# Kernel tuning notes

Measured on AMD Instinct MI355X. Metric: run time of the kernel, lower is better.

Reference implementation:

```python
import jax, jax.numpy as jnp
import numpy as np

# ---- static configuration (matches init_kwargs) ----
B = 8; CIN = 3; COUT = 3
H_IN, W_IN = 128, 256          # img_size
H, W = 32, 64                  # internal grid = img_size / scale_factor
E = 256; HID = 512             # embed_dim, mlp hidden (ratio 2)
NR, NPHI = 3, 4                # DISCO kernel_shape
K = 1 + (NR - 1) * NPHI        # 9 piecewise-linear basis functions
LMAX = MMAX = H                # SHT truncation on internal grid
PI = np.pi

# ---- DISCO basis: psi[k, ho, hi, dlon] (quadrature folded in), stored as conj(rfft) over lon ----
def _build_psi(nlat_in, nlon_in, nlat_out, cutoff):
    ti = PI * (np.arange(nlat_in) + 0.5) / nlat_in
    to = PI * (np.arange(nlat_out) + 0.5) / nlat_out
    ph = 2 * PI * np.arange(nlon_in) / nlon_in
    cto, sto = np.cos(to)[:, None, None], np.sin(to)[:, None, None]
    cti, sti = np.cos(ti)[None, :, None], np.sin(ti)[None, :, None]
    cph, sph = np.cos(ph)[None, None, :], np.sin(ph)[None, None, :]
    r = np.arccos(np.clip(cto * cti + sto * sti * cph, -1.0, 1.0))      # great-circle dist
    alpha = np.arctan2(sti * sph, cti * sto - sti * cto * cph)          # azimuth
    dr = cutoff / (NR - 1); dphi = 2 * PI / NPHI
    quad = (sti * (PI / nlat_in) * (2 * PI / nlon_in)) * (r <= cutoff)  # quadrature * cutoff mask
    psi = np.empty((K, nlat_out, nlat_in, nlon_in), np.float32)
    psi[0] = np.clip(1 - r / dr, 0, 1) * quad                           # isotropic center basis
    for j in range(1, NR):
        tr = np.clip(1 - np.abs(r - j * dr) / dr, 0, 1)
        for k in range(NPHI):
            d = np.abs(np.mod(alpha - k * dphi + PI, 2 * PI) - PI)
            psi[1 + (j - 1) * NPHI + k] = tr * np.clip(1 - d / dphi, 0, 1) * quad
    return np.conj(np.fft.rfft(psi, axis=-1)).astype(np.complex64)

PSIH_ENC = jnp.asarray(_build_psi(H_IN, W_IN, H, 4 * PI / (H - 1)))
PSIH_INT = jnp.asarray(_build_psi(H, W, H, 4 * (NR + 1) * PI / (H - 1)))
PSIH_DEC = jnp.asarray(_build_psi(H_IN, W_IN, H_IN, 4 * PI / (H - 1)))

# ---- normalized associated Legendre for SHT on internal equiangular grid ----
def _legendre(lmax, theta):
    ct, st = np.cos(theta), np.sin(theta)
    P = np.zeros((lmax, lmax, theta.size))
    P[0, 0] = 1.0 / np.sqrt(2.0)
    for m in range(1, lmax):
        P[m, m] = np.sqrt((2 * m + 1) / (2.0 * m)) * st * P[m - 1, m - 1]
    for m in range(lmax - 1):
        P[m + 1, m] = np.sqrt(2 * m + 3.0) * ct * P[m, m]
    for m in range(lmax):
        for l in range(m + 2, lmax):
            a = np.sqrt((4.0 * l * l - 1) / (l * l - m * m))
            b = a * np.sqrt(((l - 1.0) ** 2 - m * m) / (4.0 * (l - 1) ** 2 - 1))
            P[l, m] = a * ct * P[l - 1, m] - b * P[l - 2, m]
    return P  # [l, m, h]

_THETA = PI * (np.arange(H) + 0.5) / H
_P = _legendre(LMAX, _THETA).astype(np.float32)
PW = jnp.asarray(_P * (np.sin(_THETA) * (PI / H))[None, None, :])  # analysis (with quadrature)
PT = jnp.asarray(_P)                                                # synthesis

# ---- bilinear resample (32,64)->(128,256), periodic in lon ----
_fi = np.clip((np.arange(H_IN) + 0.5) * H / H_IN - 0.5, 0, H - 1)
LAT_I0 = jnp.asarray(np.floor(_fi).astype(np.int32))
LAT_I1 = jnp.asarray(np.minimum(np.floor(_fi).astype(np.int32) + 1, H - 1))
LAT_W = jnp.asarray((_fi - np.floor(_fi)).astype(np.float32))
_fj = np.arange(W_IN) * W / W_IN
LON_J0 = jnp.asarray((np.floor(_fj).astype(np.int32)) % W)
LON_J1 = jnp.asarray((np.floor(_fj).astype(np.int32) + 1) % W)
LON_W = jnp.asarray((_fj - np.floor(_fj)).astype(np.float32))


def _disco(x, psih, n_in, stride):
    # circular cross-correlation over lon via FFT: z[b,c,k,ho,wo]
    Xh = jnp.fft.rfft(x, axis=-1)
    Zh = jnp.einsum('khim,bcim->bckhm', psih, Xh)
    return jnp.fft.irfft(Zh, n=n_in, axis=-1)[..., ::stride]


def _spectral(x, w):
    # driscoll-healy spectral conv: per-l channel mixing in SH space
    Xh = jnp.fft.rfft(x, axis=-1)[..., :MMAX]
    c = jnp.einsum('lmh,bchm->bclm', PW, Xh)
    c = jnp.einsum('ocl,bclm->bolm', w, c)
    Xo = jnp.einsum('lmh,bolm->bohm', PT, c)
    Xo = jnp.pad(Xo, ((0, 0), (0, 0), (0, 0), (0, W // 2 + 1 - MMAX)))
    return jnp.fft.irfft(Xo, n=W, axis=-1)


def _resample(x):
    a = jnp.take(x, LAT_I0, axis=2) * (1 - LAT_W)[:, None] + jnp.take(x, LAT_I1, axis=2) * LAT_W[:, None]
    return jnp.take(a, LON_J0, axis=3) * (1 - LON_W) + jnp.take(a, LON_J1, axis=3) * LON_W


def _forward(x, enc_w, lconv_w, gconv_w, mlp_w1, mlp_b1, mlp_w2, mlp_b2, skip_w, skip_b, dec_w):
    # encoder: DISCO conv (128,256)->(32,64), CIN->E
    z = _disco(x, PSIH_ENC, W_IN, W_IN // W)          # [B,CIN,K,32,64]
    x = jnp.einsum('ock,bckhw->bohw', enc_w, z)       # [B,E,32,64]
    for i in range(4):
        res = x
        if i % 2 == 0:  # local DISCO block
            z = _disco(x, PSIH_INT, W, 1)
            x = jnp.einsum('ock,bckhw->bohw', lconv_w[i // 2], z)
        else:           # global spectral (SHT) block
            x = _spectral(x, gconv_w[i // 2])
        # MLP (1x1 convs) + linear outer skip (norm = Identity)
        h = jax.nn.relu(jnp.einsum('oc,bchw->bohw', mlp_w1[i], x) + mlp_b1[i][:, None, None])
        x = jnp.einsum('oc,bchw->bohw', mlp_w2[i], h) + mlp_b2[i][:, None, None]
        x = x + jnp.einsum('oc,bchw->bohw', skip_w[i], res) + skip_b[i][:, None, None]
    # decoder: bilinear upsample then DISCO conv at full res, E->COUT (mix channels first: COUT small)
    x = _resample(x)                                  # [B,E,128,256]
    u = jnp.einsum('ock,bchw->bokhw', dec_w, x)       # [B,COUT,K,128,256]
    Uh = jnp.fft.rfft(u, axis=-1)
    Yh = jnp.einsum('khim,bokim->bohm', PSIH_DEC, Uh)
    return jnp.fft.irfft(Yh, n=W_IN, axis=-1)         # [B,COUT,128,256]


def setup_inputs() -> dict:
    key = jax.random.key(0)
    ks = jax.random.split(key, 8)
    f = jnp.float32
    return dict(
        x=jax.random.normal(ks[0], (B, CIN, H_IN, W_IN), f),
        enc_w=jax.random.normal(ks[1], (E, CIN, K), f) * float(1 / np.sqrt(CIN * K)),
        lconv_w=jax.random.normal(ks[2], (2, E, E, K), f) * float(1 / np.sqrt(E * K)),
        gconv_w=jax.random.normal(ks[3], (2, E, E, LMAX), f) * float(1 / np.sqrt(E)),
        mlp_w1=jax.random.normal(ks[4], (4, HID, E), f) * float(np.sqrt(2.0 / E)),
        mlp_b1=jnp.zeros((4, HID), f),
        mlp_w2=jax.random.normal(ks[5], (4, E, HID), f) * float(1 / np.sqrt(HID)),
        mlp_b2=jnp.zeros((4, E), f),
        skip_w=jax.random.normal(ks[6], (4, E, E), f) * float(np.sqrt(0.5 / E)),
        skip_b=jnp.zeros((4, E), f),
        dec_w=jax.random.normal(ks[7], (COUT, E, K), f) * float(1 / np.sqrt(E * K)),
    )


def reference(x, enc_w, lconv_w, gconv_w, mlp_w1, mlp_b1, mlp_w2, mlp_b2, skip_w, skip_b, dec_w):
    return _forward(x, enc_w, lconv_w, gconv_w, mlp_w1, mlp_b1, mlp_w2, mlp_b2, skip_w, skip_b, dec_w)
```

## Files before the change

### kernel.cpp

```cpp
#include <hip/hip_runtime.h>
#include <math.h>
#include <utility>

#define DI __device__ __forceinline__

namespace {

typedef unsigned short u16;
typedef unsigned int u32;
using f16x8 = __attribute__((ext_vector_type(8))) _Float16;
using f32x4 = __attribute__((ext_vector_type(4))) float;

constexpr int BB  = 8;
constexpr int CIN = 3;
constexpr int HIN = 128, WIN = 256;
constexpr int EE  = 256;
constexpr int NSP = BB * 32 * 64;
constexpr double PI_D = 3.14159265358979323846;
constexpr int ME_ENC = 5120, ME_INT = 2048, ME_DEC = 4608;
constexpr int HW_E = 34;

DI u16 f16rne(float x) { _Float16 h = (_Float16)x; return __builtin_bit_cast(unsigned short, h); }
DI float f16tof(u16 u) { return (float)__builtin_bit_cast(_Float16, u); }
DI u32 packhl(float v) {
  u16 h = f16rne(v);
  u16 l = f16rne(v - f16tof(h));
  return (u32)h | ((u32)l << 16);
}

DI bool psi_point(int nlat_in, int nlon_in, int nlat_out, double cutoff,
                  int ho, int hi, int d, bool wantv, float* out9)
{
  double ti = PI_D * (hi + 0.5) / nlat_in;
  double to = PI_D * (ho + 0.5) / nlat_out;
  double ph = 2.0 * PI_D * d / nlon_in;
  double cto = cos(to), sto = sin(to);
  double cti = cos(ti), sti = sin(ti);
  double cph = cos(ph), sph = sin(ph);
  double ca = cto * cti + sto * sti * cph;
  ca = fmin(1.0, fmax(-1.0, ca));
  double r = acos(ca);
  if (r > cutoff) return false;
  if (wantv) {
    double dr   = cutoff * 0.5;
    double dphi = PI_D * 0.5;
    double quad = sti * (PI_D / nlat_in) * (2.0 * PI_D / nlon_in);
    out9[0] = (float)(fmin(1.0, fmax(0.0, 1.0 - r / dr)) * quad);
    double alpha = atan2(sti * sph, cti * sto - sti * cto * cph);
#pragma unroll
    for (int j = 1; j <= 2; ++j) {
      double tr = fmin(1.0, fmax(0.0, 1.0 - fabs(r - j * dr) / dr));
#pragma unroll
      for (int k2 = 0; k2 < 4; ++k2) {
        double xx = alpha - k2 * dphi + PI_D;
        double yy = xx - 2.0 * PI_D * floor(xx / (2.0 * PI_D));
        double dd = fabs(yy - PI_D);
        out9[1 + (j - 1) * 4 + k2] = (float)(tr * fmin(1.0, fmax(0.0, 1.0 - dd / dphi)) * quad);
      }
    }
  }
  return true;
}

__global__ void k_psi_count(int nlat_in, int nlon_in, int nlat_out, double cutoff, int* cnt)
{
  int hi = blockIdx.x, ho = blockIdx.y, d = threadIdx.x;
  float dummy[9];
  bool in = psi_point(nlat_in, nlon_in, nlat_out, cutoff, ho, hi, d, false, dummy);
  unsigned long long mask = __ballot(in);
  if ((threadIdx.x & 63) == 0) {
    int tot = __popcll(mask);
    if (tot) atomicAdd(cnt + ho * nlat_in + hi, tot);
  }
}

__global__ void k_psi_scan(int nlat_in, int maxe, int* cnt, int* offs)
{
  int ho = blockIdx.x;
  int* c = cnt + ho * nlat_in;
  int* o = offs + ho * (nlat_in + 1);
  int run = 0;
  for (int hi = 0; hi < nlat_in; ++hi) {
    o[hi] = run < maxe ? run : maxe;
    run += c[hi];
    c[hi] = 0;
  }
  o[nlat_in] = run < maxe ? run : maxe;
}

__global__ void k_psi_fill(int nlat_in, int nlon_in, int nlat_out, double cutoff,
                           int maxe, int* cnt, const int* __restrict__ offs, float* __restrict__ tab)
{
  int hi = blockIdx.x, ho = blockIdx.y, d = threadIdx.x;
  float p9[9];
  bool in = psi_point(nlat_in, nlon_in, nlat_out, cutoff, ho, hi, d, true, p9);
  unsigned long long mask = __ballot(in);
  int lane = threadIdx.x & 63;
  int tot = __popcll(mask);
  int wbase = 0;
  if (lane == 0 && tot) wbase = atomicAdd(cnt + ho * nlat_in + hi, tot);
  wbase = __shfl(wbase, 0, 64);
  if (in) {
    int rank = __popcll(mask & ((1ull << lane) - 1ull));
    int idx = offs[ho * (nlat_in + 1) + hi] + wbase + rank;
    if (idx < maxe) {
      float* te = tab + ((size_t)ho * maxe + idx) * 12;
      te[0] = __int_as_float((hi << 16) | d);
#pragma unroll
      for (int k = 0; k < 9; ++k) te[1 + k] = p9[k];
      te[10] = 0.f; te[11] = 0.f;
    }
  }
}

__global__ void k_legendre(float* __restrict__ PW, float* __restrict__ PT)
{
  int h = threadIdx.x;
  if (h >= 32) return;
  double th = PI_D * (h + 0.5) / 32.0;
  double ct = cos(th), st = sin(th);
  double quad = st * (PI_D / 32.0);
  double diag = 0.70710678118654752440;
  for (int m = 0; m < 32; ++m) {
    if (m > 0) diag = sqrt((2.0 * m + 1.0) / (2.0 * m)) * st * diag;
    double plm2 = diag;
    PT[((size_t)m * 32 + m) * 32 + h] = (float)plm2;
    PW[((size_t)m * 32 + m) * 32 + h] = (float)(plm2 * quad);
    if (m + 1 < 32) {
      double plm1 = sqrt(2.0 * m + 3.0) * ct * diag;
      PT[((size_t)(m + 1) * 32 + m) * 32 + h] = (float)plm1;
      PW[((size_t)(m + 1) * 32 + m) * 32 + h] = (float)(plm1 * quad);
      for (int l = m + 2; l < 32; ++l) {
        double a  = sqrt((4.0 * l * l - 1.0) / ((double)l * l - (double)m * m));
        double bb = a * sqrt((((double)(l - 1) * (l - 1)) - (double)m * m) /
                             (4.0 * (double)(l - 1) * (l - 1) - 1.0));
        double p = a * ct * plm1 - bb * plm2;
        PT[((size_t)l * 32 + m) * 32 + h] = (float)p;
        PW[((size_t)l * 32 + m) * 32 + h] = (float)(p * quad);
        plm2 = plm1; plm1 = p;
      }
    }
    for (int l = 0; l < m; ++l) {
      PT[((size_t)l * 32 + m) * 32 + h] = 0.f;
      PW[((size_t)l * 32 + m) * 32 + h] = 0.f;
    }
  }
}

__global__ void k_tw2(float* tc256, float* ts256, float* tc64, float* ts64)
{
  int t = threadIdx.x;
  double th = 2.0 * PI_D * t / 256.0;
  tc256[t] = (float)cos(th);
  ts256[t] = (float)sin(th);
  if (t < 64) {
    double th2 = 2.0 * PI_D * t / 64.0;
    tc64[t] = (float)cos(th2);
    ts64[t] = (float)sin(th2);
  }
}

__global__ void k_twmat(u32* __restrict__ tw256, u32* __restrict__ itw256,
                        u32* __restrict__ tw64, u32* __restrict__ itw64,
                        u32* __restrict__ iffold)
{
  int t = blockIdx.x * 256 + threadIdx.x;
  if (t < 256 * 129) {
    int w = t / 129, m = t % 129;
    double th = 2.0 * PI_D * ((m * w) & 255) / 256.0;
    tw256[w * 258 + 2 * m]     = packhl((float)cos(th));
    tw256[w * 258 + 2 * m + 1] = packhl((float)(-sin(th)));
  }
  if (t < 129 * 256) {
    int m = t >> 8, w = t & 255;
    double th = 2.0 * PI_D * ((m * w) & 255) / 256.0;
    float cr, ci;
    if (m == 0)        { cr = 1.f / 256.f; ci = 0.f; }
    else if (m == 128) { cr = ((w & 1) ? -1.f : 1.f) / 256.f; ci = 0.f; }
    else { cr = (float)(2.0 * cos(th) / 256.0); ci = (float)(-2.0 * sin(th) / 256.0); }
    itw256[(2 * m) * 256 + w] = packhl(cr);
    if (2 * m + 1 < 258) itw256[(2 * m + 1) * 256 + w] = packhl(ci);
  }
  if (t < 64 * 33) {
    int w = t / 33, m = t % 33;
    double th = 2.0 * PI_D * ((m * w) & 63) / 64.0;
    tw64[w * 66 + 2 * m]     = packhl((float)cos(th));
    tw64[w * 66 + 2 * m + 1] = packhl((float)(-sin(th)));
  }
  if (t < 33 * 64) {
    int m = t >> 6, w = t & 63;
    double th = 2.0 * PI_D * ((m * w) & 63) / 64.0;
    float cr, ci;
    if (m == 0)       { cr = 1.f / 64.f; ci = 0.f; }
    else if (m == 32) { cr = ((w & 1) ? -1.f : 1.f) / 64.f; ci = 0.f; }
    else { cr = (float)(2.0 * cos(th) / 64.0); ci = (float)(-2.0 * sin(th) / 64.0); }
    itw64[(2 * m) * 64 + w] = packhl(cr);
    if (2 * m + 1 < 66) itw64[(2 * m + 1) * 64 + w] = packhl(ci);
  }
  if (t < 129 * 64) {
    int m = t >> 6, wo = t & 63;
    double th = 2.0 * PI_D * ((m * wo) & 63) / 64.0;
    float cr, ci;
    if (m == 0)        { cr = 1.f / 256.f; ci = 0.f; }
    else if (m == 128) { cr = 1.f / 256.f; ci = 0.f; }
    else { cr = (float)(2.0 * cos(th) / 256.0); ci = (float)(-2.0 * sin(th) / 256.0); }
    iffold[(2 * m) * 64 + wo] = packhl(cr);
    if (2 * m + 1 < 258) iffold[(2 * m + 1) * 64 + wo] = packhl(ci);
  }
}

__global__ __launch_bounds__(256) void k_split(const float* __restrict__ in,
                                               u32* __restrict__ out, int n)
{
  for (int i = blockIdx.x * 256 + threadIdx.x; i < n; i += gridDim.x * 256)
    out[i] = packhl(in[i]);
}

__global__ void k_gwT_lp(const float* __restrict__ gw, u32* __restrict__ gwTlp)
{
  int idx = blockIdx.x * 256 + threadIdx.x;
  int c = idx & 255, o = (idx >> 8) & 255, l = idx >> 16;
  gwTlp[idx] = packhl(gw[((size_t)o * 256 + c) * 32 + l]);
}

__global__ void k_decT(const float* __restrict__ dw, float* __restrict__ dt)
{
  int idx = blockIdx.x * 256 + threadIdx.x;
  if (idx >= 27 * 256) return;
  int c = idx & 255, ok = idx >> 8;
  int o = ok / 9, k = ok % 9;
  dt[idx] = dw[((size_t)o * 256 + c) * 9 + k];
}

__global__ __launch_bounds__(320) void k_psih_dec(const int* __restrict__ off,
    const float* __restrict__ tab, const float* __restrict__ tc, const float* __restrict__ ts,
    float* __restrict__ psih)
{
  int ho = blockIdx.x, hw = blockIdx.y;
  int hi = ho - 16 + hw;
  int t = threadIdx.x;
  if (t >= 258) return;
  int m = t >> 1, ri = t & 1;
  const float* tw = ri ? ts : tc;
  float acc[9] = {};
  if (hi >= 0 && hi < 128) {
    int e0 = off[ho * 129 + hi], e1 = off[ho * 129 + hi + 1];
    const float* tb = tab + ((size_t)ho * ME_DEC + e0) * 12;
    for (int e = e0; e < e1; ++e, tb += 12) {
      int d = __float_as_int(tb[0]) & 0xffff;
      float v = tw[(m * d) & 255];
#pragma unroll
      for (int k = 0; k < 9; ++k) acc[k] += tb[1 + k] * v;
    }
  }
  size_t base = ((size_t)(ho * 33 + hw) * 9) * 258 + 2 * m + ri;
#pragma unroll
  for (int k = 0; k < 9; ++k) psih[base + (size_t)k * 258] = acc[k];
}

__global__ __launch_bounds__(128) void k_psih_int(const int* __restrict__ off,
    const float* __restrict__ tab, const float* __restrict__ tc, const float* __restrict__ ts,
    float* __restrict__ psih)
{
  int ho = blockIdx.x, hi = blockIdx.y;
  int t = threadIdx.x;
  if (t >= 66) return;
  int m = t >> 1, ri = t & 1;
  const float* tw = ri ? ts : tc;
  float acc[9] = {};
  int e0 = off[ho * 33 + hi], e1 = off[ho * 33 + hi + 1];
  const float* tb = tab + ((size_t)ho * ME_INT + e0) * 12;
  for (int e = e0; e < e1; ++e, tb += 12) {
    int d = __float_as_int(tb[0]) & 0xffff;
    float v = tw[(m * d) & 63];
#pragma unroll
    for (int k = 0; k < 9; ++k) acc[k] += tb[1 + k] * v;
  }
  size_t base = ((size_t)(ho * 32 + hi) * 9) * 66 + 2 * m + ri;
#pragma unroll
  for (int k = 0; k < 9; ++k) psih[base + (size_t)k * 66] = acc[k];
}

__global__ __launch_bounds__(320) void k_psih_enc(const int* __restrict__ off,
    const float* __restrict__ tab, const float* __restrict__ tc, const float* __restrict__ ts,
    float* __restrict__ psih)
{
  int ho = blockIdx.x, hw = blockIdx.y;
  int hi = 4 * ho - 15 + hw;
  int t = threadIdx.x;
  if (t >= 258) return;
  int m = t >> 1, ri = t & 1;
  const float* tw = ri ? ts : tc;
  float acc[9] = {};
  if (hi >= 0 && hi < 128) {
    int e0 = off[ho * 129 + hi], e1 = off[ho * 129 + hi + 1];
    const float* tb = tab + ((size_t)ho * ME_ENC + e0) * 12;
    for (int e = e0; e < e1; ++e, tb += 12) {
      int d = __float_as_int(tb[0]) & 0xffff;
      float v = tw[(m * d) & 255];
#pragma unroll
      for (int k = 0; k < 9; ++k) acc[k] += tb[1 + k] * v;
    }
  }
  size_t base = ((size_t)(ho * HW_E + hw) * 9) * 258 + 2 * m + ri;
#pragma unroll
  for (int k = 0; k < 9; ++k) psih[base + (size_t)k * 258] = acc[k];
}

__global__ __launch_bounds__(192) void k_enc_mconv(const float* __restrict__ psih,
    const float* __restrict__ XhE, float* __restrict__ Zh)
{
  int ho = blockIdx.x, cb = blockIdx.y;
  int c = cb >> 3, b = cb & 7;
  int m = threadIdx.x;
  if (m > 128) return;
  const float2* X2 = (const float2*)XhE;
  const float2* P2 = (const float2*)psih;
  float zr[9] = {}, zi[9] = {};
  int hi0 = 4 * ho - 15;
  for (int hw = 0; hw < HW_E; ++hw) {
    int hi = hi0 + hw;
    if (hi < 0 || hi > 127) continue;
    float2 xv = X2[((size_t)(b * 3 + c) * 128 + hi) * 129 + m];
    size_t pb = ((size_t)(ho * HW_E + hw) * 9) * 129 + m;
#pragma unroll
    for (int k = 0; k < 9; ++k) {
      float2 p = P2[pb + (size_t)k * 129];
      zr[k] += p.x * xv.x - p.y * xv.y;
      zi[k] += p.x * xv.y + p.y * xv.x;
    }
  }
#pragma unroll
  for (int k = 0; k < 9; ++k)
    ((float2*)Zh)[(((size_t)(c * 9 + k) * 8 + b) * 32 + ho) * 129 + m] =
        make_float2(zr[k], zi[k]);
}

__global__ __launch_bounds__(320) void k_int_mconv(const float* __restrict__ xh,
    const float* __restrict__ psih, float* __restrict__ zh, int c0)
{
  int ho = blockIdx.x, g = blockIdx.y, b = blockIdx.z;
  int t = threadIdx.x;
  if (t >= 264) return;
  int cl = t / 33, m = t % 33;
  int c = c0 + g * 8 + cl;
  const float2* X2 = (const float2*)xh;
  const float2* P2 = (const float2*)psih;
  float zr[9] = {}, zi[9] = {};
  for (int hi = 0; hi < 32; ++hi) {
    float2 xv = X2[((size_t)(c * 8 + b) * 32 + hi) * 33 + m];
    size_t pb = ((size_t)(ho * 32 + hi) * 9) * 33 + m;
#pragma unroll
    for (int k = 0; k < 9; ++k) {
      float2 p = P2[pb + (size_t)k * 33];
      zr[k] += p.x * xv.x - p.y * xv.y;
      zi[k] += p.x * xv.y + p.y * xv.x;
    }
  }
  int crow = (g * 8 + cl) * 9;
#pragma unroll
  for (int k = 0; k < 9; ++k)
    ((float2*)zh)[((size_t)(crow + k)) * 8448 + b * 1056 + ho * 33 + m] =
        make_float2(zr[k], zi[k]);
}

__global__ __launch_bounds__(192) void k_dec_mconv(const float* __restrict__ psih,
    const float* __restrict__ gh, float* __restrict__ yh)
{
  int ho = blockIdx.x, b = blockIdx.y;
  int m = threadIdx.x;
  if (m > 128) return;
  const float2* P2 = (const float2*)psih;
  const float2* G2 = (const float2*)gh;
  float yr[3] = {}, yi[3] = {};
  for (int hw = 0; hw < 33; ++hw) {
    int hi = ho - 16 + hw;
    if (hi < 0 || hi > 127) continue;
    size_t pb = ((size_t)(ho * 33 + hw) * 9) * 129 + m;
#pragma unroll
    for (int k = 0; k < 9; ++k) {
      float2 p = P2[pb + (size_t)k * 129];
#pragma unroll
      for (int o = 0; o < 3; ++o) {
        float2 gv = G2[((size_t)((o * 9 + k) * 8 + b) * 128 + hi) * 129 + m];
        yr[o] += p.x * gv.x - p.y * gv.y;
        yi[o] += p.x * gv.y + p.y * gv.x;
      }
    }
  }
#pragma unroll
  for (int o = 0; o < 3; ++o)
    ((float2*)yh)[((size_t)(b * 3 + o) * 128 + ho) * 129 + m] = make_float2(yr[o], yi[o]);
}

__global__ __launch_bounds__(64) void k_analysis2(const float* __restrict__ PW,
    const float* __restrict__ XH, u32* __restrict__ c1sp)
{
  int c = blockIdx.x, b = blockIdx.y;
  int t = threadIdx.x;
  __shared__ float s[32 * 64];
  __shared__ float pwl[32 * 33];
  const float* xr = XH + ((size_t)(c * 8 + b) * 32) * 66;
  for (int h = 0; h < 32; ++h) s[h * 64 + t] = xr[h * 66 + t];
  int m = t >> 1;
  for (int l = 0; l < 32; ++l) {
    __syncthreads();
#pragma unroll
    for (int j = 0; j < 16; ++j) {
      int idx = t * 16 + j;
      pwl[(idx >> 5) * 33 + (idx & 31)] = PW[(size_t)l * 1024 + idx];
    }
    __syncthreads();
    float acc = 0.f;
#pragma unroll
    for (int h = 0; h < 32; ++h) acc += pwl[m * 33 + h] * s[h * 64 + t];
    c1sp[(size_t)l * 131072 + c * 512 + b * 64 + t] = packhl(acc);
  }
}

__global__ __launch_bounds__(64) void k_synth2(const float* __restrict__ PT,
    const float* __restrict__ c2s, float* __restrict__ Xo)
{
  int o = blockIdx.x, b = blockIdx.y;
  int t = threadIdx.x;
  __shared__ float s2[32 * 64];
  __shared__ float ptl[32 * 33];
  for (int l = 0; l < 32; ++l)
    s2[l * 64 + t] = c2s[((size_t)(l * 256 + o)) * 512 + b * 64 + t];
  int m = t >> 1;
  float acc[32];
#pragma unroll
  for (int h = 0; h < 32; ++h) acc[h] = 0.f;
  for (int l = 0; l < 32; ++l) {
    __syncthreads();
#pragma unroll
    for (int j = 0; j < 16; ++j) {
      int idx = t * 16 + j;
      ptl[(idx >> 5) * 33 + (idx & 31)] = PT[(size_t)l * 1024 + idx];
    }
    __syncthreads();
    float sv = s2[l * 64 + t];
#pragma unroll
    for (int h = 0; h < 32; ++h) acc[h] += ptl[m * 33 + h] * sv;
  }
  size_t base = ((size_t)(o * 8 + b) * 32) * 64 + t;
#pragma unroll
  for (int h = 0; h < 32; ++h) Xo[base + (size_t)h * 64] = acc[h];
}

__global__ __launch_bounds__(256) void k_gemm(
    int M, int N, int K,
    const float* __restrict__ A, const u32* __restrict__ Ap, int lda, long long sA,
    const float* __restrict__ Bm, const u32* __restrict__ Bp, int ldb, long long sB,
    float* __restrict__ C, int ldc, long long sC, u32* __restrict__ Cp,
    const float* __restrict__ bias, int flags)
{
  if (A)  A  += (size_t)blockIdx.z * sA;
  if (Ap) Ap += (size_t)blockIdx.z * sA;
  if (Bm) Bm += (size_t)blockIdx.z * sB;
  if (Bp) Bp += (size_t)blockIdx.z * sB;
  if (C)  C  += (size_t)blockIdx.z * sC;
  if (Cp) Cp += (size_t)blockIdx.z * sC;
  __shared__ alignas(16) u16 Ah[128 * 36], Al[128 * 36], Bh[128 * 36], Bl[128 * 36];
  int bm = blockIdx.y * 128, bn = blockIdx.x * 128;
  int tid = threadIdx.x;
  int sr = tid >> 1, k2 = tid & 1;
  int lane = tid & 63, wid = tid >> 6;
  int wr = wid >> 1, wc = wid & 1;
  int lrow = lane & 15, kg = lane >> 4;
  f32x4 acc[4][4] = {};
  bool bok = (bn + sr) < N;

  for (int k0 = 0; k0 < K; k0 += 32) {
    {
      u32* ph = (u32*)&Ah[sr * 36 + k2 * 16];
      u32* pl = (u32*)&Al[sr * 36 + k2 * 16];
      if (Ap) {
        const u32* Ar = Ap + (size_t)(bm + sr) * lda + k0 + k2 * 16;
#pragma unroll
        for (int j2 = 0; j2 < 8; ++j2) {
          int gk = k0 + k2 * 16 + 2 * j2;
          u32 w0 = (gk < K)     ? Ar[2 * j2]     : 0u;
          u32 w1 = (gk + 1 < K) ? Ar[2 * j2 + 1] : 0u;
          ph[j2] = (w0 & 0xffffu) | (w1 << 16);
          pl[j2] = (w0 >> 16) | (w1 & 0xffff0000u);
        }
      } else {
        const float* Ar = A + (size_t)(bm + sr) * lda + k0 + k2 * 16;
#pragma unroll
        for (int j2 = 0; j2 < 8; ++j2) {
          int gk = k0 + k2 * 16 + 2 * j2;
          float v0 = (gk < K)     ? Ar[2 * j2]     : 0.f;
          float v1 = (gk + 1 < K) ? Ar[2 * j2 + 1] : 0.f;
          u16 h0 = f16rne(v0), h1 = f16rne(v1);
          u16 l0 = f16rne(v0 - f16tof(h0)), l1 = f16rne(v1 - f16tof(h1));
          ph[j2] = (u32)h0 | ((u32)h1 << 16);
          pl[j2] = (u32)l0 | ((u32)l1 << 16);
        }
      }
    }
    {
      u32* ph = (u32*)&Bh[sr * 36 + k2 * 16];
      u32* pl = (u32*)&Bl[sr * 36 + k2 * 16];
      if (Bp) {
        const u32* Bc = Bp + bn + sr;
#pragma unroll
        for (int j2 = 0; j2 < 8; ++j2) {
          int gk = k0 + k2 * 16 + 2 * j2;
          u32 w0 = (bok && gk < K)     ? Bc[(size_t)gk * ldb]       : 0u;
          u32 w1 = (bok && gk + 1 < K) ? Bc[(size_t)(gk + 1) * ldb] : 0u;
          ph[j2] = (w0 & 0xffffu) | (w1 << 16);
          pl[j2] = (w0 >> 16) | (w1 & 0xffff0000u);
        }
      } else {
        const float* Bc = Bm + bn + sr;
#pragma unroll
        for (int j2 = 0; j2 < 8; ++j2) {
          int gk = k0 + k2 * 16 + 2 * j2;
          float v0 = (bok && gk < K)     ? Bc[(size_t)gk * ldb]       : 0.f;
          float v1 = (bok && gk + 1 < K) ? Bc[(size_t)(gk + 1) * ldb] : 0.f;
          u16 h0 = f16rne(v0), h1 = f16rne(v1);
          u16 l0 = f16rne(v0 - f16tof(h0)), l1 = f16rne(v1 - f16tof(h1));
          ph[j2] = (u32)h0 | ((u32)h1 << 16);
          pl[j2] = (u32)l0 | ((u32)l1 << 16);
        }
      }
    }
    __syncthreads();
    f16x8 fah[4], fal[4], fbh[4], fbl[4];
#pragma unroll
    for (int i = 0; i < 4; ++i) {
      int ar = wr * 64 + i * 16 + lrow;
      fah[i] = *(const f16x8*)&Ah[ar * 36 + kg * 8];
      fal[i] = *(const f16x8*)&Al[ar * 36 + kg * 8];
      int br = wc * 64 + i * 16 + lrow;
      fbh[i] = *(const f16x8*)&Bh[br * 36 + kg * 8];
      fbl[i] = *(const f16x8*)&Bl[br * 36 + kg * 8];
    }
#pragma unroll
    for (int i = 0; i < 4; ++i)
#pragma unroll
      for (int j = 0; j < 4; ++j) {
        acc[i][j] = __builtin_amdgcn_mfma_f32_16x16x32_f16(fah[i], fbh[j], acc[i][j], 0, 0, 0);
        acc[i][j] = __builtin_amdgcn_mfma_f32_16x16x32_f16(fah[i], fbl[j], acc[i][j], 0, 0, 0);
        acc[i][j] = __builtin_amdgcn_mfma_f32_16x16x32_f16(fal[i], fbh[j], acc[i][j], 0, 0, 0);
      }
    __syncthreads();
  }

#pragma unroll
  for (int i = 0; i < 4; ++i) {
    int gm0 = bm + wr * 64 + i * 16 + kg * 4;
#pragma unroll
    for (int j = 0; j < 4; ++j) {
      int gn = bn + wc * 64 + j * 16 + lrow;
      if (gn >= N) continue;
#pragma unroll
      for (int rr = 0; rr < 4; ++rr) {
        int gm = gm0 + rr;
        size_t idx = (size_t)gm * ldc + gn;
        float v = acc[i][j][rr];
        if (flags & 4) v += bias[gm];
        if (flags & 2) v += C[idx];
        if (flags & 1) v = fmaxf(v, 0.f);
        if (C) C[idx] = v;
        if (flags & 8) Cp[idx] = packhl(v);
      }
    }
  }
}

__global__ __launch_bounds__(256) void k_gemm_m27(const float* __restrict__ A,
    const float* __restrict__ Bm, float* __restrict__ C)
{
  int n = blockIdx.x * 256 + threadIdx.x;
  float acc[27] = {};
  for (int k = 0; k < 256; ++k) {
    float bv = Bm[(size_t)k * NSP + n];
#pragma unroll
    for (int m = 0; m < 27; ++m) acc[m] += A[m * 256 + k] * bv;
  }
#pragma unroll
  for (int m = 0; m < 27; ++m) C[(size_t)m * NSP + n] = acc[m];
}

__global__ __launch_bounds__(256) void k_resample(const float* __restrict__ gi, float* __restrict__ gf)
{
  int t = blockIdx.x * 256 + threadIdx.x;
  int WO = t & 255, HO = (t >> 8) & 127, b = (t >> 15) & 7, ok = t >> 18;
  float fi = fminf(fmaxf(HO * 0.25f - 0.375f, 0.f), 31.f);
  int i0 = (int)fi;
  int i1 = min(i0 + 1, 31);
  float wi = fi - (float)i0;
  int j0 = WO >> 2;
  int j1 = (j0 + 1) & 63;
  float wj = (float)(WO & 3) * 0.25f;
  const float* s = gi + (size_t)ok * NSP + b * 2048;
  float v00 = s[i0 * 64 + j0], v01 = s[i0 * 64 + j1];
  float v10 = s[i1 * 64 + j0], v11 = s[i1 * 64 + j1];
  float a0 = v00 * (1.f - wj) + v01 * wj;
  float a1 = v10 * (1.f - wj) + v11 * wj;
  gf[((size_t)ok * 8 + b) * 32768 + HO * 256 + WO] = a0 * (1.f - wi) + a1 * wi;
}

}

extern "C" void kernel_launch(void* const* d_in, const int* in_sizes, int n_in,
                              void* d_out, int out_size, void* d_ws, size_t ws_size,
                              hipStream_t stream)
{
  const float* x_in  = (const float*)d_in[0];
  const float* enc_w = (const float*)d_in[1];
  const float* lconv = (const float*)d_in[2];
  const float* gconv = (const float*)d_in[3];
  const float* w1    = (const float*)d_in[4];
  const float* b1    = (const float*)d_in[5];
  const float* w2    = (const float*)d_in[6];
  const float* b2    = (const float*)d_in[7];
  const float* skw   = (const float*)d_in[8];
  const float* skb   = (const float*)d_in[9];
  const float* decw  = (const float*)d_in[10];
  float* out = (float*)d_out;

  char* ws = (char*)d_ws;
  size_t off = 0;
  auto alloc = [&](size_t nfloats) -> float* {
    float* p = (float*)(ws + off);
    off += ((nfloats * 4 + 255) / 256) * 256;
    return p;
  };
  float* PW    = alloc(32768);
  float* PT    = alloc(32768);
  float* tc256 = alloc(256);
  float* ts256 = alloc(256);
  float* tc64  = alloc(64);
  float* ts64  = alloc(64);
  u32* TW256p  = (u32*)alloc(256 * 258);
  u32* ITW256p = (u32*)alloc(258 * 256);
  u32* TW64p   = (u32*)alloc(64 * 66);
  u32* ITW64p  = (u32*)alloc(66 * 64);
  u32* IFp     = (u32*)alloc(258 * 64);
  int*   cnt2  = (int*)alloc(21504);
  int*   cnt_enc = cnt2;
  int*   cnt_int = cnt2 + 4096;
  int*   cnt_dec = cnt2 + 5120;
  int*   off_enc = (int*)alloc(32 * 129);
  int*   off_int = (int*)alloc(32 * 33);
  int*   off_dec = (int*)alloc(128 * 129);
  float* decT     = alloc(27 * 256);
  float* psih_dec = alloc((size_t)128 * 33 * 9 * 258);
  float* psih_int = alloc((size_t)32 * 32 * 9 * 66);
  float* psih_enc = alloc((size_t)32 * HW_E * 9 * 258);
  u32* enc_wp = (u32*)alloc(256 * 27);
  u32* w1p    = (u32*)alloc(4 * 512 * 256);
  u32* w2p    = (u32*)alloc(4 * 256 * 512);
  u32* skwp   = (u32*)alloc(4 * 256 * 256);
  u32* lconvp = (u32*)alloc(2 * 256 * 2304);
  float* P  = alloc((size_t)EE * NSP);
  float* Q  = alloc((size_t)EE * NSP);
  float* T  = alloc((size_t)EE * NSP);
  u32*   Tp = (u32*)alloc((size_t)EE * NSP);
  float* U  = alloc(19005440);
  (void)ws_size; (void)in_sizes; (void)n_in; (void)out_size;

  float* tab_dec = U;
  float* tab_int = U + 7077888;
  float* tab_enc = U + 7864320;
  float* zc      = U;
  float* XhE     = U + 442368;
  float* ZhE     = U + 1234944;
  float* XH      = U;
  float* ZH      = U + 4325376;
  float* XO      = U + 14057472;
  u32*   gwTlp   = (u32*)U;
  u32*   c1sp    = (u32*)(U + 2097152);
  float* c2s     = U + 6291456;
  float* Xo_s    = U + 10485760;
  float* XHs     = U + 14680064;
  u32*   Hbp     = (u32*)U;
  u32*   Pp      = (u32*)(U + 8388608);
  float* g_int   = U;
  float* g_full  = U + 524288;
  float* GH      = U + 7602176;
  float* YH      = U + 14735360;

  const double CUT_LOC = 4.0 * PI_D / 31.0;
  const double CUT_INT = 16.0 * PI_D / 31.0;
  auto splitN = [&](const float* src, u32* dst, int n) {
    int g = (n + 255) / 256; if (g > 2048) g = 2048;
    hipLaunchKernelGGL(k_split, dim3(g), dim3(256), 0, stream, src, dst, n);
  };
  const float* F0 = nullptr; const u32* U0 = nullptr; u32* W0 = nullptr;

  hipMemsetAsync(cnt2, 0, 21504 * 4, stream);
  hipLaunchKernelGGL(k_legendre, dim3(1), dim3(64), 0, stream, PW, PT);
  hipLaunchKernelGGL(k_tw2, dim3(1), dim3(256), 0, stream, tc256, ts256, tc64, ts64);
  hipLaunchKernelGGL(k_twmat, dim3(129), dim3(256), 0, stream, TW256p, ITW256p, TW64p, ITW64p, IFp);
  hipLaunchKernelGGL(k_decT, dim3(27), dim3(256), 0, stream, decw, decT);
  splitN(enc_w, enc_wp, 256 * 27);
  splitN(w1,    w1p,    4 * 512 * 256);
  splitN(w2,    w2p,    4 * 256 * 512);
  splitN(skw,   skwp,   4 * 256 * 256);
  splitN(lconv, lconvp, 2 * 256 * 2304);

  hipLaunchKernelGGL(k_psi_count, dim3(128, 32), dim3(256), 0, stream, 128, 256, 32, CUT_LOC, cnt_enc);
  hipLaunchKernelGGL(k_psi_scan,  dim3(32), dim3(1), 0, stream, 128, ME_ENC, cnt_enc, off_enc);
  hipLaunchKernelGGL(k_psi_fill,  dim3(128, 32), dim3(256), 0, stream, 128, 256, 32, CUT_LOC, ME_ENC, cnt_enc, off_enc, tab_enc);

  hipLaunchKernelGGL(k_psi_count, dim3(32, 32), dim3(64), 0, stream, 32, 64, 32, CUT_INT, cnt_int);
  hipLaunchKernelGGL(k_psi_scan,  dim3(32), dim3(1), 0, stream, 32, ME_INT, cnt_int, off_int);
  hipLaunchKernelGGL(k_psi_fill,  dim3(32, 32), dim3(64), 0, stream, 32, 64, 32, CUT_INT, ME_INT, cnt_int, off_int, tab_int);

  hipLaunchKernelGGL(k_psi_count, dim3(128, 128), dim3(256), 0, stream, 128, 256, 128, CUT_LOC, cnt_dec);
  hipLaunchKernelGGL(k_psi_scan,  dim3(128), dim3(1), 0, stream, 128, ME_DEC, cnt_dec, off_dec);
  hipLaunchKernelGGL(k_psi_fill,  dim3(128, 128), dim3(256), 0, stream, 128, 256, 128, CUT_LOC, ME_DEC, cnt_dec, off_dec, tab_dec);

  hipLaunchKernelGGL(k_psih_dec, dim3(128, 33), dim3(320), 0, stream, off_dec, tab_dec, tc256, ts256, psih_dec);
  hipLaunchKernelGGL(k_psih_int, dim3(32, 32),  dim3(128), 0, stream, off_int, tab_int, tc64, ts64, psih_int);
  hipLaunchKernelGGL(k_psih_enc, dim3(32, HW_E), dim3(320), 0, stream, off_enc, tab_enc, tc256, ts256, psih_enc);

  hipLaunchKernelGGL(k_gemm, dim3(3, 24, 1), dim3(256), 0, stream,
                     3072, 258, 256, x_in, U0, 256, 0LL, F0, TW256p, 258, 0LL,
                     XhE, 258, 0LL, W0, F0, 0);
  hipLaunchKernelGGL(k_enc_mconv, dim3(32, 24), dim3(192), 0, stream, psih_enc, XhE, ZhE);
  hipLaunchKernelGGL(k_gemm, dim3(1, 54, 1), dim3(256), 0, stream,
                     6912, 64, 258, ZhE, U0, 258, 0LL, F0, IFp, 64, 0LL,
                     zc, 64, 0LL, W0, F0, 0);
  hipLaunchKernelGGL(k_gemm, dim3(128, 2, 1), dim3(256), 0, stream,
                     256, NSP, 27, F0, enc_wp, 27, 0LL, zc, U0, NSP, 0LL,
                     P, NSP, 0LL, W0, F0, 0);

  for (int i = 0; i < 4; ++i) {
    int layer = i >> 1;
    if ((i & 1) == 0) {
      hipLaunchKernelGGL(k_gemm, dim3(1, 512, 1), dim3(256), 0, stream,
                         65536, 66, 64, P, U0, 64, 0LL, F0, TW64p, 66, 0LL,
                         XH, 66, 0LL, W0, F0, 0);
      for (int cc = 0; cc < 4; ++cc) {
        hipLaunchKernelGGL(k_int_mconv, dim3(32, 8, 8), dim3(320), 0, stream,
                           XH, psih_int, ZH, cc * 64);
        hipLaunchKernelGGL(k_gemm, dim3(132, 2, 1), dim3(256), 0, stream,
                           256, 16896, 576,
                           F0, lconvp + (size_t)layer * 589824 + cc * 576, 2304, 0LL,
                           ZH, U0, 16896, 0LL,
                           XO, 16896, 0LL, W0, F0, cc ? 2 : 0);
      }
      hipLaunchKernelGGL(k_gemm, dim3(1, 512, 1), dim3(256), 0, stream,
                         65536, 64, 66, XO, U0, 66, 0LL, F0, ITW64p, 64, 0LL,
                         T, 64, 0LL, Tp, F0, 8);
    } else {
      hipLaunchKernelGGL(k_gwT_lp, dim3(8192), dim3(256), 0, stream,
                         gconv + (size_t)layer * 2097152, gwTlp);
      hipLaunchKernelGGL(k_gemm, dim3(1, 512, 1), dim3(256), 0, stream,
                         65536, 66, 64, P, U0, 64, 0LL, F0, TW64p, 66, 0LL,
                         XHs, 66, 0LL, W0, F0, 0);
      hipLaunchKernelGGL(k_analysis2, dim3(256, 8), dim3(64), 0, stream, PW, XHs, c1sp);
      hipLaunchKernelGGL(k_gemm, dim3(4, 2, 32), dim3(256), 0, stream,
                         256, 512, 256,
                         F0, gwTlp, 256, 65536LL, F0, c1sp, 512, 131072LL,
                         c2s, 512, 131072LL, W0, F0, 0);
      hipLaunchKernelGGL(k_synth2, dim3(256, 8), dim3(64), 0, stream, PT, c2s, Xo_s);
      hipLaunchKernelGGL(k_gemm, dim3(1, 512, 1), dim3(256), 0, stream,
                         65536, 64, 64, Xo_s, U0, 64, 0LL, F0, ITW64p, 64, 0LL,
                         T, 64, 0LL, Tp, F0, 8);
    }
    hipLaunchKernelGGL(k_gemm, dim3(128, 4, 1), dim3(256), 0, stream,
                       512, NSP, 256, F0, w1p + (size_t)i * 131072, 256, 0LL,
                       F0, Tp, NSP, 0LL,
                       (float*)nullptr, NSP, 0LL, Hbp, b1 + (size_t)i * 512, 1 | 4 | 8);
    hipLaunchKernelGGL(k_gemm, dim3(128, 2, 1), dim3(256), 0, stream,
                       256, NSP, 512, F0, w2p + (size_t)i * 131072, 512, 0LL,
                       F0, Hbp, NSP, 0LL,
                       Q, NSP, 0LL, W0, b2 + (size_t)i * 256, 4);
    splitN(P, Pp, EE * NSP);
    hipLaunchKernelGGL(k_gemm, dim3(128, 2, 1), dim3(256), 0, stream,
                       256, NSP, 256, F0, skwp + (size_t)i * 65536, 256, 0LL,
                       F0, Pp, NSP, 0LL,
                       Q, NSP, 0LL, W0, skb + (size_t)i * 256, 2 | 4);
    std::swap(P, Q);
  }

  hipLaunchKernelGGL(k_gemm_m27, dim3(64), dim3(256), 0, stream, decT, P, g_int);
  hipLaunchKernelGGL(k_resample, dim3(27648), dim3(256), 0, stream, g_int, g_full);
  hipLaunchKernelGGL(k_gemm, dim3(3, 216, 1), dim3(256), 0, stream,
                     27648, 258, 256, g_full, U0, 256, 0LL, F0, TW256p, 258, 0LL,
                     GH, 258, 0LL, W0, F0, 0);
  hipLaunchKernelGGL(k_dec_mconv, dim3(128, 8), dim3(192), 0, stream, psih_dec, GH, YH);
  hipLaunchKernelGGL(k_gemm, dim3(2, 24, 1), dim3(256), 0, stream,
                     3072, 256, 258, YH, U0, 258, 0LL, F0, ITW256p, 256, 0LL,
                     out, 256, 0LL, W0, F0, 0);
}
```

Measured before the change: 4.655 ms.

## Fuse MLP second layer with skip GEMM and batch-reuse decoder psi loads

Packs the second MLP weight and the skip weight into one K=768 matrix, with pre-summed biases, so a single GEMM reads the hidden activations and the split skip input together. This replaces two GEMMs and the read-modify-write of Q. It assumes the split skip input sits directly after the hidden buffer in memory. Separately, the decoder m-convolution now has each thread loop over all 8 batches, so each psi coefficient is loaded once instead of once per batch. It also drops out-of-range latitude iterations and uses far fewer, smaller blocks, which trades occupancy and register pressure for less memory traffic.

```diff
diff --git a/kernel.cpp b/kernel.cpp
--- a/kernel.cpp
+++ b/kernel.cpp
@@ -216,6 +216,19 @@
     out[i] = packhl(in[i]);
 }
 
+__global__ __launch_bounds__(256) void k_mergew(const float* __restrict__ w2,
+    const float* __restrict__ skw, const float* __restrict__ b2, const float* __restrict__ skb,
+    u32* __restrict__ wsp, float* __restrict__ bsum)
+{
+  int t = blockIdx.x * 256 + threadIdx.x;
+  if (t < 4 * 256) bsum[t] = b2[t] + skb[t];
+  if (t >= 4 * 256 * 768) return;
+  int k = t % 768, o = (t / 768) % 256, i = t / (768 * 256);
+  float v = (k < 512) ? w2[((size_t)i * 256 + o) * 512 + k]
+                      : skw[((size_t)i * 256 + o) * 256 + (k - 512)];
+  wsp[t] = packhl(v);
+}
+
 __global__ void k_gwT_lp(const float* __restrict__ gw, u32* __restrict__ gwTlp)
 {
   int idx = blockIdx.x * 256 + threadIdx.x;
@@ -364,33 +377,43 @@
         make_float2(zr[k], zi[k]);
 }
 
-__global__ __launch_bounds__(192) void k_dec_mconv(const float* __restrict__ psih,
+__global__ __launch_bounds__(96) void k_dec_mconv(const float* __restrict__ psih,
     const float* __restrict__ gh, float* __restrict__ yh)
 {
-  int ho = blockIdx.x, b = blockIdx.y;
-  int m = threadIdx.x;
-  if (m > 128) return;
+  int bx = blockIdx.x;
+  int ho = ((bx & 7) << 4) | (bx >> 3);
+  int mh = blockIdx.y;
+  int m = mh * 65 + threadIdx.x;
+  if (m > 128 || (mh == 0 && threadIdx.x >= 65)) return;
   const float2* P2 = (const float2*)psih;
   const float2* G2 = (const float2*)gh;
-  float yr[3] = {}, yi[3] = {};
-  for (int hw = 0; hw < 33; ++hw) {
+  float yr[8][3] = {}, yi[8][3] = {};
+  int hw0 = ho >= 16 ? 0 : 16 - ho;
+  int hw1 = ho <= 111 ? 33 : 144 - ho;
+  for (int hw = hw0; hw < hw1; ++hw) {
     int hi = ho - 16 + hw;
-    if (hi < 0 || hi > 127) continue;
     size_t pb = ((size_t)(ho * 33 + hw) * 9) * 129 + m;
+    size_t gb = (size_t)hi * 129 + m;
 #pragma unroll
     for (int k = 0; k < 9; ++k) {
       float2 p = P2[pb + (size_t)k * 129];
 #pragma unroll
       for (int o = 0; o < 3; ++o) {
-        float2 gv = G2[((size_t)((o * 9 + k) * 8 + b) * 128 + hi) * 129 + m];
-        yr[o] += p.x * gv.x - p.y * gv.y;
-        yi[o] += p.x * gv.y + p.y * gv.x;
+        size_t g0 = gb + ((size_t)((o * 9 + k) * 8) * 128) * 129;
+#pragma unroll
+        for (int b = 0; b < 8; ++b) {
+          float2 gv = G2[g0 + ((size_t)b * 128) * 129];
+          yr[b][o] += p.x * gv.x - p.y * gv.y;
+          yi[b][o] += p.x * gv.y + p.y * gv.x;
+        }
       }
     }
   }
 #pragma unroll
-  for (int o = 0; o < 3; ++o)
-    ((float2*)yh)[((size_t)(b * 3 + o) * 128 + ho) * 129 + m] = make_float2(yr[o], yi[o]);
+  for (int b = 0; b < 8; ++b)
+#pragma unroll
+    for (int o = 0; o < 3; ++o)
+      ((float2*)yh)[((size_t)(b * 3 + o) * 128 + ho) * 129 + m] = make_float2(yr[b][o], yi[b][o]);
 }
 
 __global__ __launch_bounds__(64) void k_analysis2(const float* __restrict__ PW,
@@ -653,8 +676,8 @@
   float* psih_enc = alloc((size_t)32 * HW_E * 9 * 258);
   u32* enc_wp = (u32*)alloc(256 * 27);
   u32* w1p    = (u32*)alloc(4 * 512 * 256);
-  u32* w2p    = (u32*)alloc(4 * 256 * 512);
-  u32* skwp   = (u32*)alloc(4 * 256 * 256);
+  u32* wsp    = (u32*)alloc(4 * 256 * 768);
+  float* bsum = alloc(4 * 256);
   u32* lconvp = (u32*)alloc(2 * 256 * 2304);
   float* P  = alloc((size_t)EE * NSP);
   float* Q  = alloc((size_t)EE * NSP);
@@ -699,8 +722,7 @@
   hipLaunchKernelGGL(k_decT, dim3(27), dim3(256), 0, stream, decw, decT);
   splitN(enc_w, enc_wp, 256 * 27);
   splitN(w1,    w1p,    4 * 512 * 256);
-  splitN(w2,    w2p,    4 * 256 * 512);
-  splitN(skw,   skwp,   4 * 256 * 256);
+  hipLaunchKernelGGL(k_mergew, dim3(3072), dim3(256), 0, stream, w2, skw, b2, skb, wsp, bsum);
   splitN(lconv, lconvp, 2 * 256 * 2304);
 
   hipLaunchKernelGGL(k_psi_count, dim3(128, 32), dim3(256), 0, stream, 128, 256, 32, CUT_LOC, cnt_enc);
@@ -768,15 +790,11 @@
                        512, NSP, 256, F0, w1p + (size_t)i * 131072, 256, 0LL,
                        F0, Tp, NSP, 0LL,
                        (float*)nullptr, NSP, 0LL, Hbp, b1 + (size_t)i * 512, 1 | 4 | 8);
-    hipLaunchKernelGGL(k_gemm, dim3(128, 2, 1), dim3(256), 0, stream,
-                       256, NSP, 512, F0, w2p + (size_t)i * 131072, 512, 0LL,
-                       F0, Hbp, NSP, 0LL,
-                       Q, NSP, 0LL, W0, b2 + (size_t)i * 256, 4);
     splitN(P, Pp, EE * NSP);
     hipLaunchKernelGGL(k_gemm, dim3(128, 2, 1), dim3(256), 0, stream,
-                       256, NSP, 256, F0, skwp + (size_t)i * 65536, 256, 0LL,
-                       F0, Pp, NSP, 0LL,
-                       Q, NSP, 0LL, W0, skb + (size_t)i * 256, 2 | 4);
+                       256, NSP, 768, F0, wsp + (size_t)i * 196608, 768, 0LL,
+                       F0, Hbp, NSP, 0LL,
+                       Q, NSP, 0LL, W0, bsum + (size_t)i * 256, 4);
     std::swap(P, Q);
   }
 
@@ -785,7 +803,7 @@
   hipLaunchKernelGGL(k_gemm, dim3(3, 216, 1), dim3(256), 0, stream,
                      27648, 258, 256, g_full, U0, 256, 0LL, F0, TW256p, 258, 0LL,
                      GH, 258, 0LL, W0, F0, 0);
-  hipLaunchKernelGGL(k_dec_mconv, dim3(128, 8), dim3(192), 0, stream, psih_dec, GH, YH);
+  hipLaunchKernelGGL(k_dec_mconv, dim3(128, 2), dim3(96), 0, stream, psih_dec, GH, YH);
   hipLaunchKernelGGL(k_gemm, dim3(2, 24, 1), dim3(256), 0, stream,
                      3072, 256, 258, YH, U0, 258, 0LL, F0, ITW256p, 256, 0LL,
                      out, 256, 0LL, W0, F0, 0);
```

Result: slower. 4.799 ms (+3.1%).
